# Kernel tuning notes

Hardware: AMD Instinct MI355X
Metric: run time of the kernel (lower is better)

Reference implementation:

```python
import jax, jax.numpy as jnp
import numpy as np

EMBED_DIM = 1024
NUM_HEADS = 16
HEAD_DIM = EMBED_DIM // NUM_HEADS


def setup_inputs() -> dict:
    key = jax.random.key(0)
    k1, k2, k3, k4, k5 = jax.random.split(key, 5)
    B, T, C = 2, 2048, EMBED_DIM
    s = 1.0 / np.sqrt(C)
    return {
        "x": jax.random.normal(k1, (B, T, C), dtype=jnp.float32),
        "W_qkv": jax.random.normal(k2, (C, 3 * C), dtype=jnp.float32) * s,
        "b_qkv": jnp.zeros((3 * C,), dtype=jnp.float32),
        "W_out": jax.random.normal(k3, (C, C), dtype=jnp.float32) * s,
        "b_out": jnp.zeros((C,), dtype=jnp.float32),
    }


def reference(x, W_qkv, b_qkv, W_out, b_out):
    B, T, C = x.shape
    H, D = NUM_HEADS, HEAD_DIM
    qkv = x @ W_qkv + b_qkv                       # [B, T, 3C]
    q, k, v = jnp.split(qkv, 3, axis=-1)
    # [B, H, T, D]
    q = q.reshape(B, T, H, D).transpose(0, 2, 1, 3)
    k = k.reshape(B, T, H, D).transpose(0, 2, 1, 3)
    v = v.reshape(B, T, H, D).transpose(0, 2, 1, 3)
    scores = jnp.einsum("bhqd,bhkd->bhqk", q, k) / np.sqrt(D)  # [B,H,T,T]
    causal = jnp.tril(jnp.ones((T, T), dtype=bool))
    scores = jnp.where(causal[None, None], scores, -jnp.inf)
    weights = jax.nn.softmax(scores, axis=-1)
    out = jnp.einsum("bhqk,bhkd->bhqd", weights, v)  # [B,H,T,D]
    out = out.transpose(0, 2, 1, 3).reshape(B, T, C)
    return out @ W_out + b_out
```

## Files before the change

### kernel.cpp

```cpp
#include <hip/hip_runtime.h>
#include <stdint.h>

typedef unsigned short u16t;
typedef __attribute__((ext_vector_type(8))) short bf16x8;
typedef __attribute__((ext_vector_type(4))) float f32x4;

#define DEV __device__ __forceinline__

DEV u16t f2bf(float f) {
  union { float f; unsigned u; } v; v.f = f;
  unsigned r = v.u + 0x7FFFu + ((v.u >> 16) & 1u);
  return (u16t)(r >> 16);
}

DEV void glds16(const void* g, void* l) {
  __builtin_amdgcn_global_load_lds((const __attribute__((address_space(1))) void*)g,
                                   (__attribute__((address_space(3))) void*)l, 16, 0, 0);
}

__global__ __launch_bounds__(256) void k_cast_x(const float* __restrict__ x,
                                                u16t* __restrict__ xb, int n) {
  int i = (blockIdx.x * 256 + threadIdx.x) * 8;
  if (i >= n) return;
  const float4* p = (const float4*)(x + i);
  float4 a = p[0], b = p[1];
  union { u16t h[8]; int4 v; } o;
  o.h[0] = f2bf(a.x); o.h[1] = f2bf(a.y); o.h[2] = f2bf(a.z); o.h[3] = f2bf(a.w);
  o.h[4] = f2bf(b.x); o.h[5] = f2bf(b.y); o.h[6] = f2bf(b.z); o.h[7] = f2bf(b.w);
  *(int4*)(xb + i) = o.v;
}

__global__ __launch_bounds__(256) void k_transpose_cast(const float* __restrict__ src,
                                                        u16t* __restrict__ dst,
                                                        int R, int C) {
  __shared__ u16t tile[64][65];
  int c0 = blockIdx.x * 64, r0 = blockIdx.y * 64;
  int tid = threadIdx.x;
#pragma unroll
  for (int i = 0; i < 16; i++) {
    int idx = tid + i * 256;
    int r = idx >> 6, c = idx & 63;
    tile[c][r] = f2bf(src[(size_t)(r0 + r) * C + (c0 + c)]);
  }
  __syncthreads();
#pragma unroll
  for (int i = 0; i < 16; i++) {
    int idx = tid + i * 256;
    int rr = idx >> 6, cc = idx & 63;
    dst[(size_t)(c0 + rr) * R + (r0 + cc)] = tile[rr][cc];
  }
}

template <int K>
DEV void gemm_mainloop(const u16t* __restrict__ A, const u16t* __restrict__ Bt,
                       int m0, int n0, u16t* ldsA, u16t* ldsB, f32x4 acc[4][4]) {
  const int tid = threadIdx.x;
  const int lane = tid & 63;
  const int wid = tid >> 6;
  const int wm = wid >> 1, wn = wid & 1;
#pragma unroll
  for (int i = 0; i < 4; i++)
#pragma unroll
    for (int j = 0; j < 4; j++) acc[i][j] = f32x4{0.f, 0.f, 0.f, 0.f};

  char* lA = (char*)ldsA;
  char* lB = (char*)ldsB;

  for (int k0 = 0; k0 < K; k0 += 32) {
#pragma unroll
    for (int j = 0; j < 2; j++) {
      int g = wid * 64 + lane + j * 256;
      int row = g >> 2;
      int cb = (g & 3) * 16;
      glds16((const char*)(A + (size_t)(m0 + row) * K + k0) + cb,
             lA + j * 4096 + wid * 1024);
      glds16((const char*)(Bt + (size_t)(n0 + row) * K + k0) + cb,
             lB + j * 4096 + wid * 1024);
    }
    __syncthreads();
    bf16x8 af[4], bfr[4];
    const int lr = lane & 15;
    const int ko = (lane >> 4) * 8;
#pragma unroll
    for (int f = 0; f < 4; f++) {
      af[f]  = *(const bf16x8*)(ldsA + (wm * 64 + f * 16 + lr) * 32 + ko);
      bfr[f] = *(const bf16x8*)(ldsB + (wn * 64 + f * 16 + lr) * 32 + ko);
    }
#pragma unroll
    for (int i = 0; i < 4; i++)
#pragma unroll
      for (int j = 0; j < 4; j++)
        acc[i][j] = __builtin_amdgcn_mfma_f32_16x16x32_bf16(af[i], bfr[j], acc[i][j], 0, 0, 0);
    __syncthreads();
  }
}

__global__ __launch_bounds__(256) void k_gemm_qkv(const u16t* __restrict__ xb,
                                                  const u16t* __restrict__ wt,
                                                  const float* __restrict__ bias,
                                                  u16t* __restrict__ q,
                                                  u16t* __restrict__ kk,
                                                  u16t* __restrict__ vt) {
  __shared__ u16t ldsA[128 * 32];
  __shared__ u16t ldsB[128 * 32];
  __shared__ u16t ldsE[4][64 * 64];
  const int m0 = blockIdx.x * 128, n0 = blockIdx.y * 128;
  f32x4 acc[4][4];
  gemm_mainloop<1024>(xb, wt, m0, n0, ldsA, ldsB, acc);

  const int lane = threadIdx.x & 63, wid = threadIdx.x >> 6;
  const int wm = wid >> 1, wn = wid & 1;
  const int nbase = n0 + wn * 64;
  const int which = nbase >> 10;
  const int hb = (nbase & 1023) >> 6;
  const int bb = m0 >> 11;
  const int t0 = (m0 & 2047) + wm * 64;
  const int bh = bb * 16 + hb;
  u16t* eb = ldsE[wid];
#pragma unroll
  for (int fm = 0; fm < 4; fm++) {
#pragma unroll
    for (int fn = 0; fn < 4; fn++) {
      float bv = bias[nbase + fn * 16 + (lane & 15)];
#pragma unroll
      for (int i = 0; i < 4; i++) {
        int t_loc = fm * 16 + (lane >> 4) * 4 + i;
        int d_loc = fn * 16 + (lane & 15);
        float v = acc[fm][fn][i] + bv;
        if (which == 2) eb[d_loc * 64 + t_loc] = f2bf(v);
        else            eb[t_loc * 64 + d_loc] = f2bf(v);
      }
    }
  }
  asm volatile("s_waitcnt lgkmcnt(0)" ::: "memory");
  u16t* dst;
  size_t base, rowstride;
  if (which == 2) { dst = vt; base = (size_t)bh * 64 * 2048 + t0; rowstride = 2048; }
  else { dst = (which == 0) ? q : kk; base = ((size_t)bh * 2048 + t0) * 64; rowstride = 64; }
#pragma unroll
  for (int it = 0; it < 8; it++) {
    int g = it * 64 + lane;
    int r = g >> 3;
    int ce = (g & 7) * 8;
    *(int4*)(dst + base + (size_t)r * rowstride + ce) = *(const int4*)(eb + r * 64 + ce);
  }
}

__global__ __launch_bounds__(256) void k_attn(const u16t* __restrict__ q,
                                              const u16t* __restrict__ kk,
                                              const u16t* __restrict__ vt,
                                              u16t* __restrict__ attn) {
  __shared__ u16t ldsK[2][64 * 64];
  __shared__ u16t ldsV[2][64 * 64];
  __shared__ u16t ldsP[4][16 * 64];
  const int p = blockIdx.x;
  const int lo = p, hi = 31 - p;
  const int bh = blockIdx.y;
  const int lane = threadIdx.x & 63, wid = threadIdx.x >> 6;
  const int lr = lane & 15, lg = lane >> 4;
  const size_t hbase = (size_t)bh * 2048 * 64;
  const size_t vbase = (size_t)bh * 64 * 2048;
  const float NINF = -__builtin_inff();
  const float CEXP = 0.1803368801111204f;

  bf16x8 qlo[2], qhi[2];
  {
    const u16t* qp  = q + hbase + (size_t)(lo * 64 + wid * 16 + lr) * 64 + lg * 8;
    const u16t* qp2 = q + hbase + (size_t)(hi * 64 + wid * 16 + lr) * 64 + lg * 8;
#pragma unroll
    for (int ks = 0; ks < 2; ks++) {
      qlo[ks] = *(const bf16x8*)(qp + ks * 32);
      qhi[ks] = *(const bf16x8*)(qp2 + ks * 32);
    }
  }

  f32x4 olo[4], ohi[4];
#pragma unroll
  for (int i = 0; i < 4; i++) {
    olo[i] = f32x4{0.f, 0.f, 0.f, 0.f};
    ohi[i] = f32x4{0.f, 0.f, 0.f, 0.f};
  }
  float mlo = NINF, llo = 0.f, mhi = NINF, lhi = 0.f;

  u16t* pb = ldsP[wid];

  auto stage = [&](int buf, int kt) {
#pragma unroll
    for (int j = 0; j < 2; j++) {
      int g = wid * 64 + lane + j * 256;
      int r = g >> 3;
      int cb = (g & 7) * 16;
      int sc = cb ^ ((r & 7) << 4);
      glds16((const char*)(kk + hbase + (size_t)(kt * 64 + r) * 64) + sc,
             (char*)ldsK[buf] + j * 4096 + wid * 1024);
      glds16((const char*)(vt + vbase + (size_t)r * 2048 + kt * 64) + sc,
             (char*)ldsV[buf] + j * 4096 + wid * 1024);
    }
  };

  auto compute = [&](int buf, bool diag, const bf16x8* qf, f32x4* o,
                     float& m_run, float& l_run) {
    const char* K = (const char*)ldsK[buf];
    const char* V = (const char*)ldsV[buf];
    float sv[4][4];
    __builtin_amdgcn_s_setprio(1);
#pragma unroll
    for (int f = 0; f < 4; f++) {
      f32x4 s = f32x4{0.f, 0.f, 0.f, 0.f};
#pragma unroll
      for (int ks = 0; ks < 2; ks++) {
        int row = f * 16 + lr;
        int cb = ks * 64 + lg * 16;
        bf16x8 kf = *(const bf16x8*)(K + row * 128 + (cb ^ ((row & 7) << 4)));
        s = __builtin_amdgcn_mfma_f32_16x16x32_bf16(kf, qf[ks], s, 0, 0, 0);
      }
#pragma unroll
      for (int i = 0; i < 4; i++) sv[f][i] = s[i];
    }
    __builtin_amdgcn_s_setprio(0);
    if (diag) {
      int qr = wid * 16 + lr;
#pragma unroll
      for (int f = 0; f < 4; f++)
#pragma unroll
        for (int i = 0; i < 4; i++)
          if (f * 16 + lg * 4 + i > qr) sv[f][i] = NINF;
    }
    float mx = sv[0][0];
#pragma unroll
    for (int f = 0; f < 4; f++)
#pragma unroll
      for (int i = 0; i < 4; i++) mx = fmaxf(mx, sv[f][i]);
    mx = fmaxf(mx, __shfl_xor(mx, 16));
    mx = fmaxf(mx, __shfl_xor(mx, 32));
    float mnew = fmaxf(m_run, mx);
    float al = exp2f((m_run - mnew) * CEXP);
    m_run = mnew;
    float ssum = 0.f;
    u16t ph[4][4];
#pragma unroll
    for (int f = 0; f < 4; f++)
#pragma unroll
      for (int i = 0; i < 4; i++) {
        float pp = exp2f((sv[f][i] - mnew) * CEXP);
        ssum += pp;
        ph[f][i] = f2bf(pp);
      }
    ssum += __shfl_xor(ssum, 16);
    ssum += __shfl_xor(ssum, 32);
    l_run = l_run * al + ssum;
#pragma unroll
    for (int df = 0; df < 4; df++)
#pragma unroll
      for (int i = 0; i < 4; i++) o[df][i] *= al;
#pragma unroll
    for (int f = 0; f < 4; f++) {
      union { u16t h[4]; uint2 v; } pk;
      pk.h[0] = ph[f][0]; pk.h[1] = ph[f][1];
      pk.h[2] = ph[f][2]; pk.h[3] = ph[f][3];
      int cby = (f * 32 + lg * 8) ^ ((lr & 7) << 4);
      *(uint2*)((char*)pb + lr * 128 + cby) = pk.v;
    }
    asm volatile("s_waitcnt lgkmcnt(0)" ::: "memory");
    __builtin_amdgcn_s_setprio(1);
#pragma unroll
    for (int ks = 0; ks < 2; ks++) {
      int cb = ks * 64 + lg * 16;
      bf16x8 pf = *(const bf16x8*)((const char*)pb + lr * 128 + (cb ^ ((lr & 7) << 4)));
#pragma unroll
      for (int df = 0; df < 4; df++) {
        int vrow = df * 16 + lr;
        bf16x8 vf = *(const bf16x8*)(V + vrow * 128 + (cb ^ ((vrow & 7) << 4)));
        o[df] = __builtin_amdgcn_mfma_f32_16x16x32_bf16(vf, pf, o[df], 0, 0, 0);
      }
    }
    __builtin_amdgcn_s_setprio(0);
  };

  stage(0, 0);
  __syncthreads();
  for (int kt = 0; kt <= hi; kt++) {
    int cur = kt & 1;
    if (kt < hi) stage(cur ^ 1, kt + 1);
    compute(cur, kt == hi, qhi, ohi, mhi, lhi);
    if (kt <= lo) compute(cur, kt == lo, qlo, olo, mlo, llo);
    __syncthreads();
  }

  const int bb = bh >> 4, h = bh & 15;
  auto epi = [&](int qt, const f32x4* o, float l_run) {
    float rinv = 1.0f / l_run;
    int t = qt * 64 + wid * 16 + lr;
    size_t rowb = ((size_t)bb * 2048 + t) * 1024 + h * 64;
#pragma unroll
    for (int df = 0; df < 4; df++) {
      union { u16t h4[4]; uint2 v; } pk;
#pragma unroll
      for (int i = 0; i < 4; i++) pk.h4[i] = f2bf(o[df][i] * rinv);
      *(uint2*)(attn + rowb + df * 16 + lg * 4) = pk.v;
    }
  };
  epi(lo, olo, llo);
  epi(hi, ohi, lhi);
}

__global__ __launch_bounds__(256) void k_gemm_out(const u16t* __restrict__ attn,
                                                  const u16t* __restrict__ wt,
                                                  const float* __restrict__ bias,
                                                  float* __restrict__ out) {
  __shared__ u16t ldsA[128 * 32];
  __shared__ u16t ldsB[128 * 32];
  const int m0 = blockIdx.x * 128, n0 = blockIdx.y * 128;
  f32x4 acc[4][4];
  gemm_mainloop<1024>(attn, wt, m0, n0, ldsA, ldsB, acc);

  const int lane = threadIdx.x & 63, wid = threadIdx.x >> 6;
  const int wm = wid >> 1, wn = wid & 1;
#pragma unroll
  for (int fm = 0; fm < 4; fm++) {
    int row = m0 + wm * 64 + fm * 16 + (lane >> 4) * 4;
#pragma unroll
    for (int fn = 0; fn < 4; fn++) {
      int col = n0 + wn * 64 + fn * 16 + (lane & 15);
      float bv = bias[col];
#pragma unroll
      for (int i = 0; i < 4; i++)
        out[(size_t)(row + i) * 1024 + col] = acc[fm][fn][i] + bv;
    }
  }
}

extern "C" void kernel_launch(void* const* d_in, const int* in_sizes, int n_in,
                              void* d_out, int out_size, void* d_ws, size_t ws_size,
                              hipStream_t stream) {
  const float* x     = (const float*)d_in[0];
  const float* W_qkv = (const float*)d_in[1];
  const float* b_qkv = (const float*)d_in[2];
  const float* W_out = (const float*)d_in[3];
  const float* b_out = (const float*)d_in[4];
  float* out = (float*)d_out;

  char* ws = (char*)d_ws;
  u16t* xb    = (u16t*)(ws);
  u16t* wqkvT = (u16t*)(ws + 8388608);
  u16t* woutT = (u16t*)(ws + 14680064);
  u16t* qb    = (u16t*)(ws + 16777216);
  u16t* kb    = (u16t*)(ws + 25165824);
  u16t* vtb   = (u16t*)(ws + 33554432);
  u16t* attnb = (u16t*)(ws + 41943040);

  k_cast_x<<<2048, 256, 0, stream>>>(x, xb, 4194304);
  k_transpose_cast<<<dim3(48, 16), 256, 0, stream>>>(W_qkv, wqkvT, 1024, 3072);
  k_transpose_cast<<<dim3(16, 16), 256, 0, stream>>>(W_out, woutT, 1024, 1024);
  k_gemm_qkv<<<dim3(32, 24), 256, 0, stream>>>(xb, wqkvT, b_qkv, qb, kb, vtb);
  k_attn<<<dim3(16, 32), 256, 0, stream>>>(qb, kb, vtb, attnb);
  k_gemm_out<<<dim3(32, 8), 256, 0, stream>>>(attnb, woutT, b_out, out);
}
```

Measured before the change: 133.2 us.

## Halve attention query tile to 32 rows, add lazy rescale and packed bf16 converts

The attention kernel now uses 128-thread blocks that each own two 32-row query tiles (paired low and high for causal balance), and twice as many blocks are launched, giving more parallelism and smaller causal tail imbalance. The online softmax skips the rescale of the running max and accumulator unless the new max exceeds the old one by a threshold, and the exponentials become fused multiply-add plus exp2. Scalar bf16 rounding is replaced by the packed v_cvt_pk_bf16_f32 instruction. The trade-off is that each K/V tile staged into LDS is reused by fewer query rows, and staging loads per thread double.

```diff
diff --git a/kernel.cpp b/kernel.cpp
--- a/kernel.cpp
+++ b/kernel.cpp
@@ -11,6 +11,12 @@
   union { float f; unsigned u; } v; v.f = f;
   unsigned r = v.u + 0x7FFFu + ((v.u >> 16) & 1u);
   return (u16t)(r >> 16);
+}
+
+DEV unsigned cvtpk(float a, float b) {
+  unsigned r;
+  asm("v_cvt_pk_bf16_f32 %0, %1, %2" : "=v"(r) : "v"(a), "v"(b));
+  return r;
 }
 
 DEV void glds16(const void* g, void* l) {
@@ -146,17 +152,20 @@
   }
 }
 
-__global__ __launch_bounds__(256) void k_attn(const u16t* __restrict__ q,
+__global__ __launch_bounds__(128) void k_attn(const u16t* __restrict__ q,
                                               const u16t* __restrict__ kk,
                                               const u16t* __restrict__ vt,
                                               u16t* __restrict__ attn) {
   __shared__ u16t ldsK[2][64 * 64];
   __shared__ u16t ldsV[2][64 * 64];
-  __shared__ u16t ldsP[4][16 * 64];
+  __shared__ u16t ldsP[2][16 * 64];
   const int p = blockIdx.x;
-  const int lo = p, hi = 31 - p;
+  const int t_lo = p, t_hi = 63 - p;
+  const int lo_tiles = (t_lo >> 1) + 1;
+  const int hi_tiles = (t_hi >> 1) + 1;
   const int bh = blockIdx.y;
-  const int lane = threadIdx.x & 63, wid = threadIdx.x >> 6;
+  const int tid = threadIdx.x;
+  const int lane = tid & 63, wid = tid >> 6;
   const int lr = lane & 15, lg = lane >> 4;
   const size_t hbase = (size_t)bh * 2048 * 64;
   const size_t vbase = (size_t)bh * 64 * 2048;
@@ -165,8 +174,8 @@
 
   bf16x8 qlo[2], qhi[2];
   {
-    const u16t* qp  = q + hbase + (size_t)(lo * 64 + wid * 16 + lr) * 64 + lg * 8;
-    const u16t* qp2 = q + hbase + (size_t)(hi * 64 + wid * 16 + lr) * 64 + lg * 8;
+    const u16t* qp  = q + hbase + (size_t)(t_lo * 32 + wid * 16 + lr) * 64 + lg * 8;
+    const u16t* qp2 = q + hbase + (size_t)(t_hi * 32 + wid * 16 + lr) * 64 + lg * 8;
 #pragma unroll
     for (int ks = 0; ks < 2; ks++) {
       qlo[ks] = *(const bf16x8*)(qp + ks * 32);
@@ -186,19 +195,19 @@
 
   auto stage = [&](int buf, int kt) {
 #pragma unroll
-    for (int j = 0; j < 2; j++) {
-      int g = wid * 64 + lane + j * 256;
+    for (int j = 0; j < 4; j++) {
+      int g = j * 128 + tid;
       int r = g >> 3;
       int cb = (g & 7) * 16;
       int sc = cb ^ ((r & 7) << 4);
       glds16((const char*)(kk + hbase + (size_t)(kt * 64 + r) * 64) + sc,
-             (char*)ldsK[buf] + j * 4096 + wid * 1024);
+             (char*)ldsK[buf] + j * 2048 + wid * 1024);
       glds16((const char*)(vt + vbase + (size_t)r * 2048 + kt * 64) + sc,
-             (char*)ldsV[buf] + j * 4096 + wid * 1024);
+             (char*)ldsV[buf] + j * 2048 + wid * 1024);
     }
   };
 
-  auto compute = [&](int buf, bool diag, const bf16x8* qf, f32x4* o,
+  auto compute = [&](int buf, bool diag, int moff, const bf16x8* qf, f32x4* o,
                      float& m_run, float& l_run) {
     const char* K = (const char*)ldsK[buf];
     const char* V = (const char*)ldsV[buf];
@@ -219,45 +228,49 @@
     }
     __builtin_amdgcn_s_setprio(0);
     if (diag) {
-      int qr = wid * 16 + lr;
+      int qr = moff + wid * 16 + lr;
 #pragma unroll
       for (int f = 0; f < 4; f++)
 #pragma unroll
         for (int i = 0; i < 4; i++)
           if (f * 16 + lg * 4 + i > qr) sv[f][i] = NINF;
     }
-    float mx = sv[0][0];
-#pragma unroll
-    for (int f = 0; f < 4; f++)
-#pragma unroll
-      for (int i = 0; i < 4; i++) mx = fmaxf(mx, sv[f][i]);
+    float m0a = fmaxf(fmaxf(sv[0][0], sv[0][1]), fmaxf(sv[0][2], sv[0][3]));
+    float m1a = fmaxf(fmaxf(sv[1][0], sv[1][1]), fmaxf(sv[1][2], sv[1][3]));
+    float m2a = fmaxf(fmaxf(sv[2][0], sv[2][1]), fmaxf(sv[2][2], sv[2][3]));
+    float m3a = fmaxf(fmaxf(sv[3][0], sv[3][1]), fmaxf(sv[3][2], sv[3][3]));
+    float mx = fmaxf(fmaxf(m0a, m1a), fmaxf(m2a, m3a));
     mx = fmaxf(mx, __shfl_xor(mx, 16));
     mx = fmaxf(mx, __shfl_xor(mx, 32));
-    float mnew = fmaxf(m_run, mx);
-    float al = exp2f((m_run - mnew) * CEXP);
-    m_run = mnew;
-    float ssum = 0.f;
-    u16t ph[4][4];
-#pragma unroll
-    for (int f = 0; f < 4; f++)
-#pragma unroll
-      for (int i = 0; i < 4; i++) {
-        float pp = exp2f((sv[f][i] - mnew) * CEXP);
-        ssum += pp;
-        ph[f][i] = f2bf(pp);
-      }
+    if (!__all(mx <= m_run + 8.0f)) {
+      float mnew = fmaxf(m_run, mx);
+      float al = exp2f((m_run - mnew) * CEXP);
+      m_run = mnew;
+      l_run *= al;
+#pragma unroll
+      for (int df = 0; df < 4; df++)
+#pragma unroll
+        for (int i = 0; i < 4; i++) o[df][i] *= al;
+    }
+    const float nmc = -m_run * CEXP;
+    float ps[4][4];
+    float fs[4];
+#pragma unroll
+    for (int f = 0; f < 4; f++) {
+#pragma unroll
+      for (int i = 0; i < 4; i++)
+        ps[f][i] = exp2f(__builtin_fmaf(sv[f][i], CEXP, nmc));
+      fs[f] = (ps[f][0] + ps[f][1]) + (ps[f][2] + ps[f][3]);
+    }
+    float ssum = (fs[0] + fs[1]) + (fs[2] + fs[3]);
     ssum += __shfl_xor(ssum, 16);
     ssum += __shfl_xor(ssum, 32);
-    l_run = l_run * al + ssum;
-#pragma unroll
-    for (int df = 0; df < 4; df++)
-#pragma unroll
-      for (int i = 0; i < 4; i++) o[df][i] *= al;
+    l_run += ssum;
 #pragma unroll
     for (int f = 0; f < 4; f++) {
-      union { u16t h[4]; uint2 v; } pk;
-      pk.h[0] = ph[f][0]; pk.h[1] = ph[f][1];
-      pk.h[2] = ph[f][2]; pk.h[3] = ph[f][3];
+      union { unsigned u[2]; uint2 v; } pk;
+      pk.u[0] = cvtpk(ps[f][0], ps[f][1]);
+      pk.u[1] = cvtpk(ps[f][2], ps[f][3]);
       int cby = (f * 32 + lg * 8) ^ ((lr & 7) << 4);
       *(uint2*)((char*)pb + lr * 128 + cby) = pk.v;
     }
@@ -279,29 +292,29 @@
 
   stage(0, 0);
   __syncthreads();
-  for (int kt = 0; kt <= hi; kt++) {
+  for (int kt = 0; kt < hi_tiles; kt++) {
     int cur = kt & 1;
-    if (kt < hi) stage(cur ^ 1, kt + 1);
-    compute(cur, kt == hi, qhi, ohi, mhi, lhi);
-    if (kt <= lo) compute(cur, kt == lo, qlo, olo, mlo, llo);
+    if (kt + 1 < hi_tiles) stage(cur ^ 1, kt + 1);
+    compute(cur, kt == (t_hi >> 1), (t_hi & 1) << 5, qhi, ohi, mhi, lhi);
+    if (kt < lo_tiles) compute(cur, kt == (t_lo >> 1), (t_lo & 1) << 5, qlo, olo, mlo, llo);
     __syncthreads();
   }
 
   const int bb = bh >> 4, h = bh & 15;
   auto epi = [&](int qt, const f32x4* o, float l_run) {
     float rinv = 1.0f / l_run;
-    int t = qt * 64 + wid * 16 + lr;
+    int t = qt * 32 + wid * 16 + lr;
     size_t rowb = ((size_t)bb * 2048 + t) * 1024 + h * 64;
 #pragma unroll
     for (int df = 0; df < 4; df++) {
-      union { u16t h4[4]; uint2 v; } pk;
-#pragma unroll
-      for (int i = 0; i < 4; i++) pk.h4[i] = f2bf(o[df][i] * rinv);
+      union { unsigned u[2]; uint2 v; } pk;
+      pk.u[0] = cvtpk(o[df][0] * rinv, o[df][1] * rinv);
+      pk.u[1] = cvtpk(o[df][2] * rinv, o[df][3] * rinv);
       *(uint2*)(attn + rowb + df * 16 + lg * 4) = pk.v;
     }
   };
-  epi(lo, olo, llo);
-  epi(hi, ohi, lhi);
+  epi(t_lo, olo, llo);
+  epi(t_hi, ohi, lhi);
 }
 
 __global__ __launch_bounds__(256) void k_gemm_out(const u16t* __restrict__ attn,
@@ -353,6 +366,6 @@
   k_transpose_cast<<<dim3(48, 16), 256, 0, stream>>>(W_qkv, wqkvT, 1024, 3072);
   k_transpose_cast<<<dim3(16, 16), 256, 0, stream>>>(W_out, woutT, 1024, 1024);
   k_gemm_qkv<<<dim3(32, 24), 256, 0, stream>>>(xb, wqkvT, b_qkv, qb, kb, vtb);
-  k_attn<<<dim3(16, 32), 256, 0, stream>>>(qb, kb, vtb, attnb);
+  k_attn<<<dim3(32, 32), 128, 0, stream>>>(qb, kb, vtb, attnb);
   k_gemm_out<<<dim3(32, 8), 256, 0, stream>>>(attnb, woutT, b_out, out);
 }
```

New measurement: 133.3 us. No clear change (+0.1%).
